# Kernel tuning notes

Hardware: AMD Instinct MI355X
Metric: run time of the kernel (lower is better)

## Reference

```python
import jax, jax.numpy as jnp
import numpy as np

H_IMG, W_IMG = 32, 32   # image_size -> seq_len = 1024
NH, HD, D = 8, 32, 256  # num_heads, head_dim, d_model
B = 8


def _relative_positions(h, w):
    # Swin-style relative position index table, [h*w, h*w] int32
    y = np.arange(h); x = np.arange(w)
    coords = np.stack(np.meshgrid(y, x, indexing='ij')).reshape(2, -1)  # [2, S]
    rel = coords[:, :, None] - coords[:, None, :]                      # [2, S, S]
    rel = rel.transpose(1, 2, 0).astype(np.int64)                      # [S, S, 2]
    rel[:, :, 0] += h - 1
    rel[:, :, 1] += w - 1
    rel[:, :, 0] *= 2 * w - 1
    return np.int32(rel.sum(-1))                                       # [S, S]

_POS = _relative_positions(H_IMG, W_IMG)


def setup_inputs() -> dict:
    key = jax.random.key(0)
    ks = jax.random.split(key, 8)
    S = H_IMG * W_IMG
    return {
        'inputs_q': jax.random.normal(ks[0], (B, S, D), jnp.float32),
        'inputs_kv': jax.random.normal(ks[1], (B, S, D), jnp.float32),
        'Wq': jax.random.normal(ks[2], (D, NH, HD), jnp.float32) / np.sqrt(D),
        'bq': jnp.zeros((NH, HD), jnp.float32),
        'Wk': jax.random.normal(ks[3], (D, NH, HD), jnp.float32) / np.sqrt(D),
        'bk': jnp.zeros((NH, HD), jnp.float32),
        'Wv': jax.random.normal(ks[4], (D, NH, HD), jnp.float32) / np.sqrt(D),
        'bv': jnp.zeros((NH, HD), jnp.float32),
        'rel_table': 0.02 * jax.random.normal(ks[5], ((2 * H_IMG - 1) * (2 * W_IMG - 1), NH), jnp.float32),
        'Wo': jax.random.normal(ks[6], (NH, HD, D), jnp.float32) / np.sqrt(NH * HD),
        'bo': jnp.zeros((D,), jnp.float32),
    }


def reference(inputs_q, inputs_kv, Wq, bq, Wk, bk, Wv, bv, rel_table, Wo, bo):
    pos = jnp.asarray(_POS)                                  # [S, S] int32 (constant)
    q = jnp.einsum('bsd,dhk->bshk', inputs_q, Wq) + bq       # [B, S, H, HD]
    k = jnp.einsum('bsd,dhk->bshk', inputs_kv, Wk) + bk
    v = jnp.einsum('bsd,dhk->bshk', inputs_kv, Wv) + bv
    q = q / jnp.sqrt(jnp.asarray(HD, q.dtype))
    attn = jnp.einsum('bqhd,bkhd->bhqk', q, k)               # [B, H, S, S]
    rel_bias = rel_table[pos]                                # [S, S, H]
    attn = attn + jnp.transpose(rel_bias, (2, 0, 1))[None]   # broadcast over batch
    attn = jax.nn.softmax(attn, axis=-1)
    x = jnp.einsum('bhqk,bkhd->bqhd', attn, v)               # [B, S, H, HD]
    return jnp.einsum('bqhd,hdf->bqf', x, Wo) + bo           # [B, S, D]
```

## Files before the change

kernel.cpp:

```cpp
#include <hip/hip_runtime.h>
#include <hip/hip_bf16.h>

#define B_SZ   8
#define S_LEN  1024
#define D_MOD  256
#define NHEADS 8
#define H_IMG  32
#define W_IMG  32
#define M_ROWS (B_SZ * S_LEN)
#define LOG2E  1.4426950408889634f
#define QSCALE_LOG2E 0.2550352766751165f

typedef _Float16 f16x8 __attribute__((ext_vector_type(8)));
typedef _Float16 f16x4 __attribute__((ext_vector_type(4)));
typedef float    f32x4 __attribute__((ext_vector_type(4)));

__global__ __launch_bounds__(256)
void wtrans_kernel(const float* __restrict__ Wq, const float* __restrict__ Wk,
                   const float* __restrict__ Wv, const float* __restrict__ Wo,
                   _Float16* __restrict__ wt) {
    const int mi = blockIdx.x >> 3;
    const int k0 = (blockIdx.x & 7) << 5;
    const float* W = (mi == 0) ? Wq : (mi == 1) ? Wk : (mi == 2) ? Wv : Wo;
    const int n = threadIdx.x;
    const float* src = W + (size_t)k0 * 256 + n;
    _Float16* dst = wt + (size_t)mi * 65536 + (size_t)n * 256 + k0;
#pragma unroll
    for (int g = 0; g < 4; ++g) {
        f16x8 o;
#pragma unroll
        for (int j = 0; j < 8; ++j) o[j] = (_Float16)src[(size_t)(g * 8 + j) * 256];
        *(f16x8*)(dst + g * 8) = o;
    }
}

__device__ inline void ldA16(const float* p, f16x8& x0, f16x8& x1) {
    f32x4 a = *(const f32x4*)p, b = *(const f32x4*)(p + 4);
    f32x4 c = *(const f32x4*)(p + 8), d = *(const f32x4*)(p + 12);
#pragma unroll
    for (int j = 0; j < 4; ++j) {
        x0[j] = (_Float16)a[j]; x0[4 + j] = (_Float16)b[j];
        x1[j] = (_Float16)c[j]; x1[4 + j] = (_Float16)d[j];
    }
}
__device__ inline void ldA16(const _Float16* p, f16x8& x0, f16x8& x1) {
    x0 = *(const f16x8*)p; x1 = *(const f16x8*)(p + 8);
}

template <typename InT, typename OutT, int VT_MODE>
__device__ inline void gemm_body(const InT* __restrict__ A, const _Float16* __restrict__ Wt,
                                 const float* __restrict__ bias, OutT* __restrict__ out,
                                 float scale, int m0, int n0) {
    __shared__ __align__(16) _Float16 As[2][64][72];
    __shared__ __align__(16) _Float16 Bt[2][64][72];
    const int tid  = threadIdx.x;
    const int w    = tid >> 6;
    const int lane = tid & 63;
    const int quad = lane >> 4;
    const int l16  = lane & 15;
    const int mq   = (w & 1) * 32;
    const int nq   = (w >> 1) * 32;

    const int srow = tid >> 2;
    const int scol = (tid & 3) << 4;
    const InT* Ap = A + (size_t)(m0 + srow) * 256 + scol;
    const _Float16* Bp = Wt + (size_t)(n0 + srow) * 256 + scol;

    f16x8 a0n, a1n, b0n, b1n;
    ldA16(Ap, a0n, a1n);
    b0n = *(const f16x8*)Bp; b1n = *(const f16x8*)(Bp + 8);
    *(f16x8*)(&As[0][srow][scol])     = a0n;
    *(f16x8*)(&As[0][srow][scol + 8]) = a1n;
    *(f16x8*)(&Bt[0][srow][scol])     = b0n;
    *(f16x8*)(&Bt[0][srow][scol + 8]) = b1n;
    __syncthreads();

    f32x4 acc[2][2];
#pragma unroll
    for (int i = 0; i < 2; ++i)
#pragma unroll
        for (int j = 0; j < 2; ++j) acc[i][j] = (f32x4){0.f, 0.f, 0.f, 0.f};

#pragma unroll
    for (int s = 0; s < 4; ++s) {
        const int cur = s & 1;
        if (s < 3) {
            ldA16(Ap + (s + 1) * 64, a0n, a1n);
            b0n = *(const f16x8*)(Bp + (s + 1) * 64);
            b1n = *(const f16x8*)(Bp + (s + 1) * 64 + 8);
        }
#pragma unroll
        for (int kk = 0; kk < 2; ++kk) {
            const int k8 = kk * 32 + quad * 8;
            f16x8 fa0 = *(const f16x8*)(&As[cur][mq + l16][k8]);
            f16x8 fa1 = *(const f16x8*)(&As[cur][mq + 16 + l16][k8]);
            f16x8 fb0 = *(const f16x8*)(&Bt[cur][nq + l16][k8]);
            f16x8 fb1 = *(const f16x8*)(&Bt[cur][nq + 16 + l16][k8]);
            acc[0][0] = __builtin_amdgcn_mfma_f32_16x16x32_f16(fa0, fb0, acc[0][0], 0, 0, 0);
            acc[0][1] = __builtin_amdgcn_mfma_f32_16x16x32_f16(fa0, fb1, acc[0][1], 0, 0, 0);
            acc[1][0] = __builtin_amdgcn_mfma_f32_16x16x32_f16(fa1, fb0, acc[1][0], 0, 0, 0);
            acc[1][1] = __builtin_amdgcn_mfma_f32_16x16x32_f16(fa1, fb1, acc[1][1], 0, 0, 0);
        }
        if (s < 3) {
            const int nxt = cur ^ 1;
            *(f16x8*)(&As[nxt][srow][scol])     = a0n;
            *(f16x8*)(&As[nxt][srow][scol + 8]) = a1n;
            *(f16x8*)(&Bt[nxt][srow][scol])     = b0n;
            *(f16x8*)(&Bt[nxt][srow][scol + 8]) = b1n;
            __syncthreads();
        }
    }

    if (VT_MODE) {
        const int b8 = (m0 >> 10) * 8;
#pragma unroll
        for (int nh = 0; nh < 2; ++nh) {
            const int col = n0 + nq + nh * 16 + l16;
            const float bv = bias[col];
#pragma unroll
            for (int mh = 0; mh < 2; ++mh) {
                const int row0 = (m0 & 1023) + mq + mh * 16 + quad * 4;
                f16x4 pk;
#pragma unroll
                for (int r = 0; r < 4; ++r) pk[r] = (_Float16)((acc[mh][nh][r] + bv) * scale);
                *(f16x4*)((_Float16*)out +
                          ((size_t)(b8 + (col >> 5)) * 32 + (col & 31)) * 1024 + row0) = pk;
            }
        }
    } else {
#pragma unroll
        for (int nh = 0; nh < 2; ++nh) {
            const int col = n0 + nq + nh * 16 + l16;
            const float bv = bias[col];
#pragma unroll
            for (int mh = 0; mh < 2; ++mh) {
#pragma unroll
                for (int r = 0; r < 4; ++r) {
                    const int row = m0 + mq + mh * 16 + quad * 4 + r;
                    out[(size_t)row * 256 + col] = (OutT)((acc[mh][nh][r] + bv) * scale);
                }
            }
        }
    }
}

__global__ __launch_bounds__(256)
void gemm_qkv_kernel(const float* __restrict__ in_q, const float* __restrict__ in_kv,
                     const _Float16* __restrict__ wt,
                     const float* __restrict__ bq, const float* __restrict__ bk,
                     const float* __restrict__ bv,
                     _Float16* __restrict__ qh, _Float16* __restrict__ kh,
                     _Float16* __restrict__ vt) {
    const int z = blockIdx.z;
    const int m0 = blockIdx.x * 64, n0 = blockIdx.y * 64;
    if (z == 0)
        gemm_body<float, _Float16, 0>(in_q, wt, bq, qh, QSCALE_LOG2E, m0, n0);
    else if (z == 1)
        gemm_body<float, _Float16, 0>(in_kv, wt + 65536, bk, kh, 1.0f, m0, n0);
    else
        gemm_body<float, _Float16, 1>(in_kv, wt + 2 * 65536, bv, vt, 1.0f, m0, n0);
}

__global__ __launch_bounds__(256)
void gemm_out_kernel(const _Float16* __restrict__ X, const _Float16* __restrict__ wt,
                     const float* __restrict__ bo, float* __restrict__ out) {
    gemm_body<_Float16, float, 0>(X, wt + (size_t)3 * 65536, bo, out, 1.0f,
                                  blockIdx.x * 64, blockIdx.y * 64);
}

__global__ __launch_bounds__(256)
void attn_kernel(const _Float16* __restrict__ q, const _Float16* __restrict__ k,
                 const _Float16* __restrict__ vt, const float* __restrict__ rel_table,
                 _Float16* __restrict__ xout) {
    __shared__ __align__(16) _Float16 Ps[4][2][32][40];
    __shared__ float bias_row[4][2][64];

    const int tid  = threadIdx.x;
    const int w    = tid >> 6;
    const int lane = tid & 63;
    const int quad = lane >> 4;
    const int l16  = lane & 15;

    const int n     = blockIdx.x;
    const int xcd   = n & 7;
    const int local = n >> 3;
    const int bh    = xcd * 8 + (local & 7);
    const int qc    = local >> 3;
    const int b     = bh >> 3, h = bh & 7;
    const int qrow_base = qc * 128 + w * 32;
    const int yq = qrow_base >> 5;

    const _Float16* qp = q + ((size_t)(b * S_LEN + qrow_base + l16)) * D_MOD + h * 32 + quad * 8;
    const f16x8 qf0 = *(const f16x8*)(qp);
    const f16x8 qf1 = *(const f16x8*)(qp + 16 * D_MOD);
    const _Float16* kp = k + ((size_t)(b * S_LEN + l16)) * D_MOD + h * 32 + quad * 8;
    const _Float16* vp = vt + ((size_t)(bh * 32 + l16)) * S_LEN + quad * 8;
    const float* bp = rel_table + ((size_t)(yq + 31) * 63 + lane) * NHEADS + h;

    f16x8 ones;
#pragma unroll
    for (int j = 0; j < 8; ++j) ones[j] = (_Float16)1.0f;

    f32x4 o00 = {0.f,0.f,0.f,0.f}, o01 = {0.f,0.f,0.f,0.f};
    f32x4 o10 = {0.f,0.f,0.f,0.f}, o11 = {0.f,0.f,0.f,0.f};
    f32x4 ol0 = {0.f,0.f,0.f,0.f}, ol1 = {0.f,0.f,0.f,0.f};

    if (lane < 63) bias_row[w][0][lane] = bp[0] * LOG2E;
    f16x8 kf0 = *(const f16x8*)(kp);
    f16x8 kf1 = *(const f16x8*)(kp + 16 * D_MOD);
    f16x8 vf0 = *(const f16x8*)(vp);
    f16x8 vf1 = *(const f16x8*)(vp + 16 * S_LEN);

    for (int kt = 0; kt < S_LEN / 32; ++kt) {
        const int cur = kt & 1, nxt = cur ^ 1;
        f16x8 nk0, nk1, nv0, nv1;
        float nb = 0.f;
        const bool more = (kt < S_LEN / 32 - 1);
        if (more) {
            const _Float16* kq = kp + (size_t)(kt + 1) * 32 * D_MOD;
            nk0 = *(const f16x8*)(kq);
            nk1 = *(const f16x8*)(kq + 16 * D_MOD);
            const _Float16* vq = vp + (kt + 1) * 32;
            nv0 = *(const f16x8*)(vq);
            nv1 = *(const f16x8*)(vq + 16 * S_LEN);
            if (lane < 63) nb = bp[-(ptrdiff_t)((kt + 1) * 63 * NHEADS)];
        }

#pragma unroll
        for (int mh = 0; mh < 2; ++mh) {
            const f16x8 qf = mh ? qf1 : qf0;
#pragma unroll
            for (int kh = 0; kh < 2; ++kh) {
                const int idx0 = mh * 16 + quad * 4 - kh * 16 - l16 + 31;
                const float* bb = &bias_row[w][cur][idx0];
                f32x4 c; c[0] = bb[0]; c[1] = bb[1]; c[2] = bb[2]; c[3] = bb[3];
                f32x4 s = __builtin_amdgcn_mfma_f32_16x16x32_f16(qf, kh ? kf1 : kf0, c, 0, 0, 0);
#pragma unroll
                for (int r = 0; r < 4; ++r)
                    Ps[w][cur][mh * 16 + quad * 4 + r][kh * 16 + l16] =
                        (_Float16)__builtin_amdgcn_exp2f(s[r]);
            }
        }

        const f16x8 pf0 = *(const f16x8*)(&Ps[w][cur][l16][quad * 8]);
        const f16x8 pf1 = *(const f16x8*)(&Ps[w][cur][16 + l16][quad * 8]);
        o00 = __builtin_amdgcn_mfma_f32_16x16x32_f16(pf0, vf0, o00, 0, 0, 0);
        o01 = __builtin_amdgcn_mfma_f32_16x16x32_f16(pf0, vf1, o01, 0, 0, 0);
        o10 = __builtin_amdgcn_mfma_f32_16x16x32_f16(pf1, vf0, o10, 0, 0, 0);
        o11 = __builtin_amdgcn_mfma_f32_16x16x32_f16(pf1, vf1, o11, 0, 0, 0);
        ol0 = __builtin_amdgcn_mfma_f32_16x16x32_f16(pf0, ones, ol0, 0, 0, 0);
        ol1 = __builtin_amdgcn_mfma_f32_16x16x32_f16(pf1, ones, ol1, 0, 0, 0);

        if (more) {
            if (lane < 63) bias_row[w][nxt][lane] = nb * LOG2E;
            kf0 = nk0; kf1 = nk1; vf0 = nv0; vf1 = nv1;
        }
    }

#pragma unroll
    for (int mh = 0; mh < 2; ++mh) {
        const f32x4 oa = mh ? o10 : o00;
        const f32x4 ob = mh ? o11 : o01;
        const f32x4 ll = mh ? ol1 : ol0;
#pragma unroll
        for (int r = 0; r < 4; ++r) {
            const float inv = __builtin_amdgcn_rcpf(ll[r]);
            const int qg = qrow_base + mh * 16 + quad * 4 + r;
            _Float16* op = xout + ((size_t)(b * S_LEN + qg)) * D_MOD + h * 32;
            op[l16]      = (_Float16)(oa[r] * inv);
            op[l16 + 16] = (_Float16)(ob[r] * inv);
        }
    }
}

extern "C" void kernel_launch(void* const* d_in, const int* in_sizes, int n_in,
                              void* d_out, int out_size, void* d_ws, size_t ws_size,
                              hipStream_t stream) {
    const float* in_q  = (const float*)d_in[0];
    const float* in_kv = (const float*)d_in[1];
    const float* Wq    = (const float*)d_in[2];
    const float* bq    = (const float*)d_in[3];
    const float* Wk    = (const float*)d_in[4];
    const float* bk    = (const float*)d_in[5];
    const float* Wv    = (const float*)d_in[6];
    const float* bv    = (const float*)d_in[7];
    const float* rel   = (const float*)d_in[8];
    const float* Wo    = (const float*)d_in[9];
    const float* bo    = (const float*)d_in[10];
    float* out = (float*)d_out;

    _Float16* qh = (_Float16*)d_ws;
    _Float16* kh = qh + (size_t)M_ROWS * D_MOD;
    _Float16* vt = kh + (size_t)M_ROWS * D_MOD;
    _Float16* xh = vt + (size_t)M_ROWS * D_MOD;
    _Float16* wt = xh + (size_t)M_ROWS * D_MOD;

    const dim3 blk(256);

    wtrans_kernel<<<dim3(32), blk, 0, stream>>>(Wq, Wk, Wv, Wo, wt);
    gemm_qkv_kernel<<<dim3(M_ROWS / 64, 4, 3), blk, 0, stream>>>(
        in_q, in_kv, wt, bq, bk, bv, qh, kh, vt);
    attn_kernel<<<dim3(512), blk, 0, stream>>>(qh, kh, vt, rel, xh);
    gemm_out_kernel<<<dim3(M_ROWS / 64, 4), blk, 0, stream>>>(xh, wt, bo, out);
}
```

Before: 142.9 us.

## Precompute per-register bias table, transpose attention MFMAs, drop LDS from GEMMs

The GEMMs now load MFMA fragments straight from global memory instead of staging tiles through double-buffered shared memory. The relative-position bias is pre-expanded, scaled by log2(e), into a per-head table laid out in MFMA accumulator order, so the attention kernel loads its bias with one vector read. The attention kernel computes the transposed products (K·Q and V·P), handles 16 query rows per wave instead of 32, and doubles the grid to 1024 blocks. This removes shared-memory traffic and barriers and raises parallelism, at the cost of redundant global loads in the GEMMs and less reuse of K/V per wave.

```diff
diff --git a/kernel.cpp b/kernel.cpp
--- a/kernel.cpp
+++ b/kernel.cpp
@@ -1,12 +1,9 @@
 #include <hip/hip_runtime.h>
-#include <hip/hip_bf16.h>
 
 #define B_SZ   8
 #define S_LEN  1024
 #define D_MOD  256
 #define NHEADS 8
-#define H_IMG  32
-#define W_IMG  32
 #define M_ROWS (B_SZ * S_LEN)
 #define LOG2E  1.4426950408889634f
 #define QSCALE_LOG2E 0.2550352766751165f
@@ -15,133 +12,50 @@
 typedef _Float16 f16x4 __attribute__((ext_vector_type(4)));
 typedef float    f32x4 __attribute__((ext_vector_type(4)));
 
+__device__ inline f16x8 cvt8(const float* p) {
+    f32x4 a = *(const f32x4*)p, b = *(const f32x4*)(p + 4);
+    f16x8 r;
+#pragma unroll
+    for (int j = 0; j < 4; ++j) { r[j] = (_Float16)a[j]; r[4 + j] = (_Float16)b[j]; }
+    return r;
+}
+
 __global__ __launch_bounds__(256)
-void wtrans_kernel(const float* __restrict__ Wq, const float* __restrict__ Wk,
-                   const float* __restrict__ Wv, const float* __restrict__ Wo,
-                   _Float16* __restrict__ wt) {
-    const int mi = blockIdx.x >> 3;
-    const int k0 = (blockIdx.x & 7) << 5;
-    const float* W = (mi == 0) ? Wq : (mi == 1) ? Wk : (mi == 2) ? Wv : Wo;
-    const int n = threadIdx.x;
-    const float* src = W + (size_t)k0 * 256 + n;
-    _Float16* dst = wt + (size_t)mi * 65536 + (size_t)n * 256 + k0;
-#pragma unroll
-    for (int g = 0; g < 4; ++g) {
-        f16x8 o;
-#pragma unroll
-        for (int j = 0; j < 8; ++j) o[j] = (_Float16)src[(size_t)(g * 8 + j) * 256];
-        *(f16x8*)(dst + g * 8) = o;
-    }
-}
-
-__device__ inline void ldA16(const float* p, f16x8& x0, f16x8& x1) {
-    f32x4 a = *(const f32x4*)p, b = *(const f32x4*)(p + 4);
-    f32x4 c = *(const f32x4*)(p + 8), d = *(const f32x4*)(p + 12);
-#pragma unroll
-    for (int j = 0; j < 4; ++j) {
-        x0[j] = (_Float16)a[j]; x0[4 + j] = (_Float16)b[j];
-        x1[j] = (_Float16)c[j]; x1[4 + j] = (_Float16)d[j];
-    }
-}
-__device__ inline void ldA16(const _Float16* p, f16x8& x0, f16x8& x1) {
-    x0 = *(const f16x8*)p; x1 = *(const f16x8*)(p + 8);
-}
-
-template <typename InT, typename OutT, int VT_MODE>
-__device__ inline void gemm_body(const InT* __restrict__ A, const _Float16* __restrict__ Wt,
-                                 const float* __restrict__ bias, OutT* __restrict__ out,
-                                 float scale, int m0, int n0) {
-    __shared__ __align__(16) _Float16 As[2][64][72];
-    __shared__ __align__(16) _Float16 Bt[2][64][72];
-    const int tid  = threadIdx.x;
-    const int w    = tid >> 6;
-    const int lane = tid & 63;
-    const int quad = lane >> 4;
-    const int l16  = lane & 15;
-    const int mq   = (w & 1) * 32;
-    const int nq   = (w >> 1) * 32;
-
-    const int srow = tid >> 2;
-    const int scol = (tid & 3) << 4;
-    const InT* Ap = A + (size_t)(m0 + srow) * 256 + scol;
-    const _Float16* Bp = Wt + (size_t)(n0 + srow) * 256 + scol;
-
-    f16x8 a0n, a1n, b0n, b1n;
-    ldA16(Ap, a0n, a1n);
-    b0n = *(const f16x8*)Bp; b1n = *(const f16x8*)(Bp + 8);
-    *(f16x8*)(&As[0][srow][scol])     = a0n;
-    *(f16x8*)(&As[0][srow][scol + 8]) = a1n;
-    *(f16x8*)(&Bt[0][srow][scol])     = b0n;
-    *(f16x8*)(&Bt[0][srow][scol + 8]) = b1n;
-    __syncthreads();
-
-    f32x4 acc[2][2];
-#pragma unroll
-    for (int i = 0; i < 2; ++i)
-#pragma unroll
-        for (int j = 0; j < 2; ++j) acc[i][j] = (f32x4){0.f, 0.f, 0.f, 0.f};
-
-#pragma unroll
-    for (int s = 0; s < 4; ++s) {
-        const int cur = s & 1;
-        if (s < 3) {
-            ldA16(Ap + (s + 1) * 64, a0n, a1n);
-            b0n = *(const f16x8*)(Bp + (s + 1) * 64);
-            b1n = *(const f16x8*)(Bp + (s + 1) * 64 + 8);
-        }
-#pragma unroll
-        for (int kk = 0; kk < 2; ++kk) {
-            const int k8 = kk * 32 + quad * 8;
-            f16x8 fa0 = *(const f16x8*)(&As[cur][mq + l16][k8]);
-            f16x8 fa1 = *(const f16x8*)(&As[cur][mq + 16 + l16][k8]);
-            f16x8 fb0 = *(const f16x8*)(&Bt[cur][nq + l16][k8]);
-            f16x8 fb1 = *(const f16x8*)(&Bt[cur][nq + 16 + l16][k8]);
-            acc[0][0] = __builtin_amdgcn_mfma_f32_16x16x32_f16(fa0, fb0, acc[0][0], 0, 0, 0);
-            acc[0][1] = __builtin_amdgcn_mfma_f32_16x16x32_f16(fa0, fb1, acc[0][1], 0, 0, 0);
-            acc[1][0] = __builtin_amdgcn_mfma_f32_16x16x32_f16(fa1, fb0, acc[1][0], 0, 0, 0);
-            acc[1][1] = __builtin_amdgcn_mfma_f32_16x16x32_f16(fa1, fb1, acc[1][1], 0, 0, 0);
-        }
-        if (s < 3) {
-            const int nxt = cur ^ 1;
-            *(f16x8*)(&As[nxt][srow][scol])     = a0n;
-            *(f16x8*)(&As[nxt][srow][scol + 8]) = a1n;
-            *(f16x8*)(&Bt[nxt][srow][scol])     = b0n;
-            *(f16x8*)(&Bt[nxt][srow][scol + 8]) = b1n;
-            __syncthreads();
-        }
-    }
-
-    if (VT_MODE) {
-        const int b8 = (m0 >> 10) * 8;
-#pragma unroll
-        for (int nh = 0; nh < 2; ++nh) {
-            const int col = n0 + nq + nh * 16 + l16;
-            const float bv = bias[col];
-#pragma unroll
-            for (int mh = 0; mh < 2; ++mh) {
-                const int row0 = (m0 & 1023) + mq + mh * 16 + quad * 4;
-                f16x4 pk;
-#pragma unroll
-                for (int r = 0; r < 4; ++r) pk[r] = (_Float16)((acc[mh][nh][r] + bv) * scale);
-                *(f16x4*)((_Float16*)out +
-                          ((size_t)(b8 + (col >> 5)) * 32 + (col & 31)) * 1024 + row0) = pk;
-            }
-        }
-    } else {
-#pragma unroll
-        for (int nh = 0; nh < 2; ++nh) {
-            const int col = n0 + nq + nh * 16 + l16;
-            const float bv = bias[col];
-#pragma unroll
-            for (int mh = 0; mh < 2; ++mh) {
-#pragma unroll
-                for (int r = 0; r < 4; ++r) {
-                    const int row = m0 + mq + mh * 16 + quad * 4 + r;
-                    out[(size_t)row * 256 + col] = (OutT)((acc[mh][nh][r] + bv) * scale);
-                }
-            }
-        }
-    }
+void prep_kernel(const float* __restrict__ Wq, const float* __restrict__ Wk,
+                 const float* __restrict__ Wv, const float* __restrict__ Wo,
+                 const float* __restrict__ rel,
+                 _Float16* __restrict__ wt, float* __restrict__ tab) {
+    if (blockIdx.x < 32) {
+        const int mi = blockIdx.x >> 3;
+        const int k0 = (blockIdx.x & 7) << 5;
+        const float* W = (mi == 0) ? Wq : (mi == 1) ? Wk : (mi == 2) ? Wv : Wo;
+        const int n = threadIdx.x;
+        const float* src = W + (size_t)k0 * 256 + n;
+        _Float16* dst = wt + (size_t)mi * 65536 + (size_t)n * 256 + k0;
+#pragma unroll
+        for (int g = 0; g < 4; ++g) {
+            f16x8 o;
+#pragma unroll
+            for (int j = 0; j < 8; ++j) o[j] = (_Float16)src[(size_t)(g * 8 + j) * 256];
+            *(f16x8*)(dst + g * 8) = o;
+        }
+        return;
+    }
+    const int flat = (blockIdx.x - 32) * 256 + threadIdx.x;
+    const int lane = flat & 63;
+    const int t1   = flat >> 6;
+    const int e    = t1 % 3;
+    const int t2   = t1 / 3;
+    const int dy31 = t2 % 63;
+    const int h    = t2 / 63;
+    const int quad = lane >> 4, l16 = lane & 15;
+    f32x4 v;
+#pragma unroll
+    for (int reg = 0; reg < 4; ++reg) {
+        const int idx = 16 * e + l16 - quad * 4 - reg + 15;
+        v[reg] = rel[(size_t)(dy31 * 63 + idx) * NHEADS + h] * LOG2E;
+    }
+    *(f32x4*)(tab + (size_t)flat * 4) = v;
 }
 
 __global__ __launch_bounds__(256)
@@ -151,71 +65,171 @@
                      const float* __restrict__ bv,
                      _Float16* __restrict__ qh, _Float16* __restrict__ kh,
                      _Float16* __restrict__ vt) {
-    const int z = blockIdx.z;
-    const int m0 = blockIdx.x * 64, n0 = blockIdx.y * 64;
-    if (z == 0)
-        gemm_body<float, _Float16, 0>(in_q, wt, bq, qh, QSCALE_LOG2E, m0, n0);
-    else if (z == 1)
-        gemm_body<float, _Float16, 0>(in_kv, wt + 65536, bk, kh, 1.0f, m0, n0);
-    else
-        gemm_body<float, _Float16, 1>(in_kv, wt + 2 * 65536, bv, vt, 1.0f, m0, n0);
-}
-
-__global__ __launch_bounds__(256)
-void gemm_out_kernel(const _Float16* __restrict__ X, const _Float16* __restrict__ wt,
-                     const float* __restrict__ bo, float* __restrict__ out) {
-    gemm_body<_Float16, float, 0>(X, wt + (size_t)3 * 65536, bo, out, 1.0f,
-                                  blockIdx.x * 64, blockIdx.y * 64);
-}
-
-__global__ __launch_bounds__(256)
-void attn_kernel(const _Float16* __restrict__ q, const _Float16* __restrict__ k,
-                 const _Float16* __restrict__ vt, const float* __restrict__ rel_table,
-                 _Float16* __restrict__ xout) {
-    __shared__ __align__(16) _Float16 Ps[4][2][32][40];
-    __shared__ float bias_row[4][2][64];
-
     const int tid  = threadIdx.x;
     const int w    = tid >> 6;
     const int lane = tid & 63;
     const int quad = lane >> 4;
     const int l16  = lane & 15;
+    const int m0 = blockIdx.x * 64, n0 = blockIdx.y * 64, z = blockIdx.z;
+    const int mq = (w & 1) * 32, nq = (w >> 1) * 32;
+
+    const float* A = z ? in_kv : in_q;
+    const float* a0p = A + (size_t)(m0 + mq + l16) * 256;
+    const float* a1p = a0p + 16 * 256;
+    const _Float16* wb = wt + (size_t)z * 65536;
+    const _Float16* b0p = wb + (size_t)(n0 + nq + l16) * 256;
+    const _Float16* b1p = b0p + 16 * 256;
+
+    f32x4 acc[2][2];
+#pragma unroll
+    for (int i = 0; i < 2; ++i)
+#pragma unroll
+        for (int j = 0; j < 2; ++j) acc[i][j] = (f32x4){0.f, 0.f, 0.f, 0.f};
+
+#pragma unroll
+    for (int kk = 0; kk < 8; ++kk) {
+        const int k8 = kk * 32 + quad * 8;
+        f16x8 fa0 = cvt8(a0p + k8);
+        f16x8 fa1 = cvt8(a1p + k8);
+        f16x8 fb0 = *(const f16x8*)(b0p + k8);
+        f16x8 fb1 = *(const f16x8*)(b1p + k8);
+        acc[0][0] = __builtin_amdgcn_mfma_f32_16x16x32_f16(fa0, fb0, acc[0][0], 0, 0, 0);
+        acc[0][1] = __builtin_amdgcn_mfma_f32_16x16x32_f16(fa0, fb1, acc[0][1], 0, 0, 0);
+        acc[1][0] = __builtin_amdgcn_mfma_f32_16x16x32_f16(fa1, fb0, acc[1][0], 0, 0, 0);
+        acc[1][1] = __builtin_amdgcn_mfma_f32_16x16x32_f16(fa1, fb1, acc[1][1], 0, 0, 0);
+    }
+
+    if (z == 2) {
+        const int b8 = (m0 >> 10) * 8;
+#pragma unroll
+        for (int nh = 0; nh < 2; ++nh) {
+            const int col = n0 + nq + nh * 16 + l16;
+            const float bvv = bv[col];
+#pragma unroll
+            for (int mh = 0; mh < 2; ++mh) {
+                const int row0 = (m0 & 1023) + mq + mh * 16 + quad * 4;
+                f16x4 pk;
+#pragma unroll
+                for (int r = 0; r < 4; ++r) pk[r] = (_Float16)(acc[mh][nh][r] + bvv);
+                *(f16x4*)(vt + ((size_t)(b8 + (col >> 5)) * 32 + (col & 31)) * 1024 + row0) = pk;
+            }
+        }
+    } else {
+        _Float16* out = z ? kh : qh;
+        const float* bias = z ? bk : bq;
+        const float scale = z ? 1.0f : QSCALE_LOG2E;
+#pragma unroll
+        for (int nh = 0; nh < 2; ++nh) {
+            const int col = n0 + nq + nh * 16 + l16;
+            const float bvv = bias[col];
+#pragma unroll
+            for (int mh = 0; mh < 2; ++mh) {
+#pragma unroll
+                for (int r = 0; r < 4; ++r) {
+                    const int row = m0 + mq + mh * 16 + quad * 4 + r;
+                    out[(size_t)row * 256 + col] = (_Float16)((acc[mh][nh][r] + bvv) * scale);
+                }
+            }
+        }
+    }
+}
+
+__global__ __launch_bounds__(256)
+void gemm_out_kernel(const _Float16* __restrict__ X, const _Float16* __restrict__ wt3,
+                     const float* __restrict__ bo, float* __restrict__ out) {
+    const int tid  = threadIdx.x;
+    const int w    = tid >> 6;
+    const int lane = tid & 63;
+    const int quad = lane >> 4;
+    const int l16  = lane & 15;
+    const int m0 = blockIdx.x * 64, n0 = blockIdx.y * 64;
+    const int mq = (w & 1) * 32, nq = (w >> 1) * 32;
+
+    const _Float16* a0p = X + (size_t)(m0 + mq + l16) * 256;
+    const _Float16* a1p = a0p + 16 * 256;
+    const _Float16* b0p = wt3 + (size_t)(n0 + nq + l16) * 256;
+    const _Float16* b1p = b0p + 16 * 256;
+
+    f32x4 acc[2][2];
+#pragma unroll
+    for (int i = 0; i < 2; ++i)
+#pragma unroll
+        for (int j = 0; j < 2; ++j) acc[i][j] = (f32x4){0.f, 0.f, 0.f, 0.f};
+
+#pragma unroll
+    for (int kk = 0; kk < 8; ++kk) {
+        const int k8 = kk * 32 + quad * 8;
+        f16x8 fa0 = *(const f16x8*)(a0p + k8);
+        f16x8 fa1 = *(const f16x8*)(a1p + k8);
+        f16x8 fb0 = *(const f16x8*)(b0p + k8);
+        f16x8 fb1 = *(const f16x8*)(b1p + k8);
+        acc[0][0] = __builtin_amdgcn_mfma_f32_16x16x32_f16(fa0, fb0, acc[0][0], 0, 0, 0);
+        acc[0][1] = __builtin_amdgcn_mfma_f32_16x16x32_f16(fa0, fb1, acc[0][1], 0, 0, 0);
+        acc[1][0] = __builtin_amdgcn_mfma_f32_16x16x32_f16(fa1, fb0, acc[1][0], 0, 0, 0);
+        acc[1][1] = __builtin_amdgcn_mfma_f32_16x16x32_f16(fa1, fb1, acc[1][1], 0, 0, 0);
+    }
+
+#pragma unroll
+    for (int nh = 0; nh < 2; ++nh) {
+        const int col = n0 + nq + nh * 16 + l16;
+        const float bvv = bo[col];
+#pragma unroll
+        for (int mh = 0; mh < 2; ++mh) {
+#pragma unroll
+            for (int r = 0; r < 4; ++r) {
+                const int row = m0 + mq + mh * 16 + quad * 4 + r;
+                out[(size_t)row * 256 + col] = acc[mh][nh][r] + bvv;
+            }
+        }
+    }
+}
+
+__global__ __launch_bounds__(256)
+void attn_kernel(const _Float16* __restrict__ q, const _Float16* __restrict__ k,
+                 const _Float16* __restrict__ vt, const float* __restrict__ tab,
+                 _Float16* __restrict__ xh) {
+    __shared__ __align__(16) _Float16 Ps[4][16][40];
+
+    const int tid  = threadIdx.x;
+    const int w    = tid >> 6;
+    const int lane = tid & 63;
+    const int quad = lane >> 4;
+    const int l16  = lane & 15;
 
     const int n     = blockIdx.x;
     const int xcd   = n & 7;
     const int local = n >> 3;
     const int bh    = xcd * 8 + (local & 7);
     const int qc    = local >> 3;
-    const int b     = bh >> 3, h = bh & 7;
-    const int qrow_base = qc * 128 + w * 32;
+    const int b = bh >> 3, h = bh & 7;
+    const int qrow_base = qc * 64 + w * 16;
     const int yq = qrow_base >> 5;
-
-    const _Float16* qp = q + ((size_t)(b * S_LEN + qrow_base + l16)) * D_MOD + h * 32 + quad * 8;
-    const f16x8 qf0 = *(const f16x8*)(qp);
-    const f16x8 qf1 = *(const f16x8*)(qp + 16 * D_MOD);
+    const int e0 = (w & 1) + 1;
+    const int e1 = (w & 1);
+
+    const f16x8 qf =
+        *(const f16x8*)(q + ((size_t)(b * S_LEN + qrow_base + l16)) * D_MOD + h * 32 + quad * 8);
     const _Float16* kp = k + ((size_t)(b * S_LEN + l16)) * D_MOD + h * 32 + quad * 8;
     const _Float16* vp = vt + ((size_t)(bh * 32 + l16)) * S_LEN + quad * 8;
-    const float* bp = rel_table + ((size_t)(yq + 31) * 63 + lane) * NHEADS + h;
+    const float* tb = tab + (size_t)h * 63 * 3 * 256 + lane * 4;
 
     f16x8 ones;
 #pragma unroll
     for (int j = 0; j < 8; ++j) ones[j] = (_Float16)1.0f;
 
-    f32x4 o00 = {0.f,0.f,0.f,0.f}, o01 = {0.f,0.f,0.f,0.f};
-    f32x4 o10 = {0.f,0.f,0.f,0.f}, o11 = {0.f,0.f,0.f,0.f};
-    f32x4 ol0 = {0.f,0.f,0.f,0.f}, ol1 = {0.f,0.f,0.f,0.f};
-
-    if (lane < 63) bias_row[w][0][lane] = bp[0] * LOG2E;
+    f32x4 o0 = {0.f,0.f,0.f,0.f}, o1 = {0.f,0.f,0.f,0.f}, ol = {0.f,0.f,0.f,0.f};
+
     f16x8 kf0 = *(const f16x8*)(kp);
     f16x8 kf1 = *(const f16x8*)(kp + 16 * D_MOD);
     f16x8 vf0 = *(const f16x8*)(vp);
     f16x8 vf1 = *(const f16x8*)(vp + 16 * S_LEN);
-
-    for (int kt = 0; kt < S_LEN / 32; ++kt) {
-        const int cur = kt & 1, nxt = cur ^ 1;
+    f32x4 c0 = *(const f32x4*)(tb + (size_t)((yq + 31) * 3 + e0) * 256);
+    f32x4 c1 = *(const f32x4*)(tb + (size_t)((yq + 31) * 3 + e1) * 256);
+
+    for (int kt = 0; kt < 32; ++kt) {
+        const bool more = (kt < 31);
         f16x8 nk0, nk1, nv0, nv1;
-        float nb = 0.f;
-        const bool more = (kt < S_LEN / 32 - 1);
+        f32x4 nc0, nc1;
         if (more) {
             const _Float16* kq = kp + (size_t)(kt + 1) * 32 * D_MOD;
             nk0 = *(const f16x8*)(kq);
@@ -223,54 +237,40 @@
             const _Float16* vq = vp + (kt + 1) * 32;
             nv0 = *(const f16x8*)(vq);
             nv1 = *(const f16x8*)(vq + 16 * S_LEN);
-            if (lane < 63) nb = bp[-(ptrdiff_t)((kt + 1) * 63 * NHEADS)];
-        }
-
-#pragma unroll
-        for (int mh = 0; mh < 2; ++mh) {
-            const f16x8 qf = mh ? qf1 : qf0;
-#pragma unroll
-            for (int kh = 0; kh < 2; ++kh) {
-                const int idx0 = mh * 16 + quad * 4 - kh * 16 - l16 + 31;
-                const float* bb = &bias_row[w][cur][idx0];
-                f32x4 c; c[0] = bb[0]; c[1] = bb[1]; c[2] = bb[2]; c[3] = bb[3];
-                f32x4 s = __builtin_amdgcn_mfma_f32_16x16x32_f16(qf, kh ? kf1 : kf0, c, 0, 0, 0);
-#pragma unroll
-                for (int r = 0; r < 4; ++r)
-                    Ps[w][cur][mh * 16 + quad * 4 + r][kh * 16 + l16] =
-                        (_Float16)__builtin_amdgcn_exp2f(s[r]);
-            }
-        }
-
-        const f16x8 pf0 = *(const f16x8*)(&Ps[w][cur][l16][quad * 8]);
-        const f16x8 pf1 = *(const f16x8*)(&Ps[w][cur][16 + l16][quad * 8]);
-        o00 = __builtin_amdgcn_mfma_f32_16x16x32_f16(pf0, vf0, o00, 0, 0, 0);
-        o01 = __builtin_amdgcn_mfma_f32_16x16x32_f16(pf0, vf1, o01, 0, 0, 0);
-        o10 = __builtin_amdgcn_mfma_f32_16x16x32_f16(pf1, vf0, o10, 0, 0, 0);
-        o11 = __builtin_amdgcn_mfma_f32_16x16x32_f16(pf1, vf1, o11, 0, 0, 0);
-        ol0 = __builtin_amdgcn_mfma_f32_16x16x32_f16(pf0, ones, ol0, 0, 0, 0);
-        ol1 = __builtin_amdgcn_mfma_f32_16x16x32_f16(pf1, ones, ol1, 0, 0, 0);
-
-        if (more) {
-            if (lane < 63) bias_row[w][nxt][lane] = nb * LOG2E;
-            kf0 = nk0; kf1 = nk1; vf0 = nv0; vf1 = nv1;
-        }
-    }
-
-#pragma unroll
-    for (int mh = 0; mh < 2; ++mh) {
-        const f32x4 oa = mh ? o10 : o00;
-        const f32x4 ob = mh ? o11 : o01;
-        const f32x4 ll = mh ? ol1 : ol0;
-#pragma unroll
-        for (int r = 0; r < 4; ++r) {
-            const float inv = __builtin_amdgcn_rcpf(ll[r]);
-            const int qg = qrow_base + mh * 16 + quad * 4 + r;
-            _Float16* op = xout + ((size_t)(b * S_LEN + qg)) * D_MOD + h * 32;
-            op[l16]      = (_Float16)(oa[r] * inv);
-            op[l16 + 16] = (_Float16)(ob[r] * inv);
-        }
-    }
+            const int dy31n = yq + 30 - kt;
+            nc0 = *(const f32x4*)(tb + (size_t)(dy31n * 3 + e0) * 256);
+            nc1 = *(const f32x4*)(tb + (size_t)(dy31n * 3 + e1) * 256);
+        }
+
+        f32x4 s0 = __builtin_amdgcn_mfma_f32_16x16x32_f16(kf0, qf, c0, 0, 0, 0);
+        f32x4 s1 = __builtin_amdgcn_mfma_f32_16x16x32_f16(kf1, qf, c1, 0, 0, 0);
+
+        f16x4 p;
+#pragma unroll
+        for (int r = 0; r < 4; ++r) p[r] = (_Float16)__builtin_amdgcn_exp2f(s0[r]);
+        *(f16x4*)(&Ps[w][l16][quad * 4]) = p;
+#pragma unroll
+        for (int r = 0; r < 4; ++r) p[r] = (_Float16)__builtin_amdgcn_exp2f(s1[r]);
+        *(f16x4*)(&Ps[w][l16][16 + quad * 4]) = p;
+
+        const f16x8 pf = *(const f16x8*)(&Ps[w][l16][quad * 8]);
+        o0 = __builtin_amdgcn_mfma_f32_16x16x32_f16(vf0, pf, o0, 0, 0, 0);
+        o1 = __builtin_amdgcn_mfma_f32_16x16x32_f16(vf1, pf, o1, 0, 0, 0);
+        ol = __builtin_amdgcn_mfma_f32_16x16x32_f16(ones, pf, ol, 0, 0, 0);
+
+        if (more) { kf0 = nk0; kf1 = nk1; vf0 = nv0; vf1 = nv1; c0 = nc0; c1 = nc1; }
+    }
+
+    const float inv = __builtin_amdgcn_rcpf(ol[0]);
+    f16x4 w0, w1;
+#pragma unroll
+    for (int r = 0; r < 4; ++r) {
+        w0[r] = (_Float16)(o0[r] * inv);
+        w1[r] = (_Float16)(o1[r] * inv);
+    }
+    _Float16* op = xh + ((size_t)(b * S_LEN + qrow_base + l16)) * D_MOD + h * 32 + quad * 4;
+    *(f16x4*)(op)      = w0;
+    *(f16x4*)(op + 16) = w1;
 }
 
 extern "C" void kernel_launch(void* const* d_in, const int* in_sizes, int n_in,
@@ -289,17 +289,19 @@
     const float* bo    = (const float*)d_in[10];
     float* out = (float*)d_out;
 
-    _Float16* qh = (_Float16*)d_ws;
-    _Float16* kh = qh + (size_t)M_ROWS * D_MOD;
-    _Float16* vt = kh + (size_t)M_ROWS * D_MOD;
-    _Float16* xh = vt + (size_t)M_ROWS * D_MOD;
-    _Float16* wt = xh + (size_t)M_ROWS * D_MOD;
+    char* wsb = (char*)d_ws;
+    _Float16* qh  = (_Float16*)(wsb);
+    _Float16* kh  = (_Float16*)(wsb + (size_t)4  * 1048576);
+    _Float16* vt  = (_Float16*)(wsb + (size_t)8  * 1048576);
+    _Float16* xh  = (_Float16*)(wsb + (size_t)12 * 1048576);
+    _Float16* wt  = (_Float16*)(wsb + (size_t)16 * 1048576);
+    float*    tab = (float*)   (wsb + (size_t)17 * 1048576);
 
     const dim3 blk(256);
 
-    wtrans_kernel<<<dim3(32), blk, 0, stream>>>(Wq, Wk, Wv, Wo, wt);
+    prep_kernel<<<dim3(410), blk, 0, stream>>>(Wq, Wk, Wv, Wo, rel, wt, tab);
     gemm_qkv_kernel<<<dim3(M_ROWS / 64, 4, 3), blk, 0, stream>>>(
         in_q, in_kv, wt, bq, bk, bv, qh, kh, vt);
-    attn_kernel<<<dim3(512), blk, 0, stream>>>(qh, kh, vt, rel, xh);
-    gemm_out_kernel<<<dim3(M_ROWS / 64, 4), blk, 0, stream>>>(xh, wt, bo, out);
-}
+    attn_kernel<<<dim3(1024), blk, 0, stream>>>(qh, kh, vt, tab, xh);
+    gemm_out_kernel<<<dim3(M_ROWS / 64, 4), blk, 0, stream>>>(xh, wt + (size_t)3 * 65536, bo, out);
+}
```

Measured after the change: 194.8 us. 1.36x slower.
